# Performance work log

Hardware: AMD Instinct MI355X
Metric: run time of the kernel (lower is better)

## Reference

```python
import jax, jax.numpy as jnp
import numpy as np

EMB = 4096
NUM_EXPERTS = 64
TOP_K = 2
TOKENS = 16384


def setup_inputs() -> dict:
    key = jax.random.key(0)
    kx, kw, kb = jax.random.split(key, 3)
    x = jax.random.normal(kx, (TOKENS, EMB), dtype=jnp.float32)
    # nn.Linear(emb_size, num_experts): weight [num_experts, emb], bias [num_experts]
    W = jax.random.normal(kw, (NUM_EXPERTS, EMB), dtype=jnp.float32) / np.sqrt(EMB)
    b = jax.random.normal(kb, (NUM_EXPERTS,), dtype=jnp.float32) * 0.01
    return {"x": x, "W": W, "b": b}


def reference(x, W, b):
    # logits = x @ W.T + b  -> [tokens, num_experts]
    logits = jnp.einsum("td,ed->te", x, W) + b
    topk_val, topk_idx = jax.lax.top_k(logits, TOP_K)  # [tokens, k]
    probs = jax.nn.softmax(topk_val, axis=-1)
    return (topk_idx, probs)
```

## Files before the change

### kernel.cpp

```cpp
#include <hip/hip_runtime.h>

#define TOKENS 16384
#define EMB 4096
#define NEXP 64
#define BK 32
#define KSP 4
#define KPER (EMB / KSP)
#define NCH (KPER / BK)

typedef __attribute__((ext_vector_type(8))) short short8;
typedef __attribute__((ext_vector_type(4))) float f32x4;
typedef __attribute__((ext_vector_type(4))) unsigned short ush4;

#define WP_USHORTS (3 * NEXP * EMB)
#define WP_FLOATS  (WP_USHORTS / 2)

__device__ __forceinline__ void gl_lds16(const void* g, void* lds) {
    __builtin_amdgcn_global_load_lds(
        (const __attribute__((address_space(1))) void*)g,
        (__attribute__((address_space(3))) void*)lds, 16, 0, 0);
}

__device__ __forceinline__ void split3(float x, unsigned short& h,
                                       unsigned short& m, unsigned short& l) {
    unsigned u = __float_as_uint(x);
    unsigned r = u + 0x7FFFu + ((u >> 16) & 1u);
    float hF = __uint_as_float(r & 0xFFFF0000u);
    h = (unsigned short)(r >> 16);
    float r1 = x - hF;
    unsigned u1 = __float_as_uint(r1);
    float mF = __uint_as_float(u1 & 0xFFFF0000u);
    m = (unsigned short)(u1 >> 16);
    float r2 = r1 - mF;
    l = (unsigned short)(__float_as_uint(r2) >> 16);
}

__device__ __forceinline__ void split3_pair(float x0, float x1,
        unsigned& hw, unsigned& mw, unsigned& lw) {
    unsigned u0 = __float_as_uint(x0), u1 = __float_as_uint(x1);
    unsigned r0 = u0 + 0x7FFFu + ((u0 >> 16) & 1u);
    unsigned r1 = u1 + 0x7FFFu + ((u1 >> 16) & 1u);
    hw = __builtin_amdgcn_perm(r1, r0, 0x07060302u);
    float s0 = x0 - __uint_as_float(r0 & 0xFFFF0000u);
    float s1 = x1 - __uint_as_float(r1 & 0xFFFF0000u);
    unsigned v0 = __float_as_uint(s0), v1 = __float_as_uint(s1);
    mw = __builtin_amdgcn_perm(v1, v0, 0x07060302u);
    float t0 = s0 - __uint_as_float(v0 & 0xFFFF0000u);
    float t1 = s1 - __uint_as_float(v1 & 0xFFFF0000u);
    lw = __builtin_amdgcn_perm(__float_as_uint(t1), __float_as_uint(t0), 0x07060302u);
}

__device__ __forceinline__ void build_frags(const float4& a0, const float4& a1,
        short8& H, short8& M, short8& L) {
    union { short8 v; unsigned u[4]; } h_, m_, l_;
    split3_pair(a0.x, a0.y, h_.u[0], m_.u[0], l_.u[0]);
    split3_pair(a0.z, a0.w, h_.u[1], m_.u[1], l_.u[1]);
    split3_pair(a1.x, a1.y, h_.u[2], m_.u[2], l_.u[2]);
    split3_pair(a1.z, a1.w, h_.u[3], m_.u[3], l_.u[3]);
    H = h_.v; M = m_.v; L = l_.v;
}

__global__ __launch_bounds__(256) void split_w(const float* __restrict__ W,
                                               unsigned short* __restrict__ Wp) {
    const int i = (blockIdx.x * 256 + threadIdx.x) * 4;
    const float4 v = *reinterpret_cast<const float4*>(W + i);
    ush4 h, m, l;
#pragma unroll
    for (int e = 0; e < 4; ++e) {
        unsigned short he, me, le;
        split3(reinterpret_cast<const float*>(&v)[e], he, me, le);
        h[e] = he; m[e] = me; l[e] = le;
    }
    *reinterpret_cast<ush4*>(Wp + i) = h;
    *reinterpret_cast<ush4*>(Wp + NEXP * EMB + i) = m;
    *reinterpret_cast<ush4*>(Wp + 2 * NEXP * EMB + i) = l;
}

#define MFMA_BLOCK(BUFC, AH0, AM0, AL0, AH1, AM1, AL1)                          \
    _Pragma("unroll")                                                           \
    for (int et = 0; et < 4; ++et) {                                            \
        const unsigned short* bp = &sB[g][BUFC][et * 16 + lr][lo * 8];          \
        const short8 bH = *reinterpret_cast<const short8*>(bp);                 \
        const short8 bM = *reinterpret_cast<const short8*>(bp + 64 * BK);       \
        const short8 bL = *reinterpret_cast<const short8*>(bp + 128 * BK);      \
        accH[0][et] = __builtin_amdgcn_mfma_f32_16x16x32_bf16(AH0, bH, accH[0][et], 0, 0, 0); \
        accL[0][et] = __builtin_amdgcn_mfma_f32_16x16x32_bf16(AH0, bM, accL[0][et], 0, 0, 0); \
        accL[0][et] = __builtin_amdgcn_mfma_f32_16x16x32_bf16(AM0, bH, accL[0][et], 0, 0, 0); \
        accL[0][et] = __builtin_amdgcn_mfma_f32_16x16x32_bf16(AM0, bM, accL[0][et], 0, 0, 0); \
        accL[0][et] = __builtin_amdgcn_mfma_f32_16x16x32_bf16(AH0, bL, accL[0][et], 0, 0, 0); \
        accL[0][et] = __builtin_amdgcn_mfma_f32_16x16x32_bf16(AL0, bH, accL[0][et], 0, 0, 0); \
        accH[1][et] = __builtin_amdgcn_mfma_f32_16x16x32_bf16(AH1, bH, accH[1][et], 0, 0, 0); \
        accL[1][et] = __builtin_amdgcn_mfma_f32_16x16x32_bf16(AH1, bM, accL[1][et], 0, 0, 0); \
        accL[1][et] = __builtin_amdgcn_mfma_f32_16x16x32_bf16(AM1, bH, accL[1][et], 0, 0, 0); \
        accL[1][et] = __builtin_amdgcn_mfma_f32_16x16x32_bf16(AM1, bM, accL[1][et], 0, 0, 0); \
        accL[1][et] = __builtin_amdgcn_mfma_f32_16x16x32_bf16(AH1, bL, accL[1][et], 0, 0, 0); \
        accL[1][et] = __builtin_amdgcn_mfma_f32_16x16x32_bf16(AL1, bH, accL[1][et], 0, 0, 0); \
    }

#define BODY(KS, AC, BUFC) do {                                                 \
    asm volatile("s_waitcnt vmcnt(4)" ::: "memory");                            \
    __builtin_amdgcn_s_barrier();                                               \
    _Pragma("unroll")                                                           \
    for (int p = 0; p < 6; ++p)                                                 \
        gl_lds16(gb[p] + ((KS) + 1) * BK,                                       \
                 &sB[g][(BUFC) ^ 1][16 * (6 * h + p)][0]);                      \
    __builtin_amdgcn_sched_barrier(0);                                          \
    short8 aH0, aM0, aL0, aH1, aM1, aL1;                                        \
    build_frags(AC[0][0], AC[0][1], aH0, aM0, aL0);                             \
    build_frags(AC[1][0], AC[1][1], aH1, aM1, aL1);                             \
    _Pragma("unroll")                                                           \
    for (int ti = 0; ti < 2; ++ti) {                                            \
        AC[ti][0] = *reinterpret_cast<const float4*>(ax[ti] + ((KS) + 2) * BK);     \
        AC[ti][1] = *reinterpret_cast<const float4*>(ax[ti] + ((KS) + 2) * BK + 4); \
    }                                                                           \
    __builtin_amdgcn_sched_barrier(0);                                          \
    MFMA_BLOCK(BUFC, aH0, aM0, aL0, aH1, aM1, aL1)                              \
} while (0)

__global__ __launch_bounds__(512) void router_fused(
    const float* __restrict__ x, const unsigned short* __restrict__ Wp,
    const float* __restrict__ b, float* __restrict__ out)
{
    __shared__ unsigned short sB[KSP][2][192][BK];

    const int t  = threadIdx.x;
    const int w  = t >> 6;
    const int l  = t & 63;
    const int g  = w >> 1;
    const int h  = w & 1;
    const int lr = l & 15;
    const int lo = l >> 4;
    const int tokB = blockIdx.x * 64;
    const int tok0 = tokB + h * 32;
    const int kb   = g * KPER;

    const float* ax[2];
    ax[0] = x + (size_t)(tok0 + lr) * EMB + kb + lo * 8;
    ax[1] = ax[0] + (size_t)16 * EMB;

    const unsigned short* gb[6];
#pragma unroll
    for (int p = 0; p < 6; ++p)
        gb[p] = Wp + (size_t)(16 * (6 * h + p) + (l >> 2)) * EMB + kb + 8 * (l & 3);

    f32x4 accH[2][4], accL[2][4];
#pragma unroll
    for (int ti = 0; ti < 2; ++ti)
#pragma unroll
        for (int et = 0; et < 4; ++et) {
            accH[ti][et] = (f32x4){0.f, 0.f, 0.f, 0.f};
            accL[ti][et] = (f32x4){0.f, 0.f, 0.f, 0.f};
        }

    float4 aA[2][2], aB[2][2];
#pragma unroll
    for (int ti = 0; ti < 2; ++ti) {
        aA[ti][0] = *reinterpret_cast<const float4*>(ax[ti]);
        aA[ti][1] = *reinterpret_cast<const float4*>(ax[ti] + 4);
    }
    __builtin_amdgcn_sched_barrier(0);
#pragma unroll
    for (int p = 0; p < 6; ++p)
        gl_lds16(gb[p], &sB[g][0][16 * (6 * h + p)][0]);
    __builtin_amdgcn_sched_barrier(0);
#pragma unroll
    for (int ti = 0; ti < 2; ++ti) {
        aB[ti][0] = *reinterpret_cast<const float4*>(ax[ti] + BK);
        aB[ti][1] = *reinterpret_cast<const float4*>(ax[ti] + BK + 4);
    }
    __builtin_amdgcn_sched_barrier(0);

#pragma unroll 1
    for (int kt = 0; kt < NCH - 2; kt += 2) {
        BODY(kt, aA, 0);
        BODY(kt + 1, aB, 1);
    }
    {
        asm volatile("s_waitcnt vmcnt(4)" ::: "memory");
        __builtin_amdgcn_s_barrier();
#pragma unroll
        for (int p = 0; p < 6; ++p)
            gl_lds16(gb[p] + (NCH - 1) * BK, &sB[g][1][16 * (6 * h + p)][0]);
        __builtin_amdgcn_sched_barrier(0);
        short8 aH0, aM0, aL0, aH1, aM1, aL1;
        build_frags(aA[0][0], aA[0][1], aH0, aM0, aL0);
        build_frags(aA[1][0], aA[1][1], aH1, aM1, aL1);
        MFMA_BLOCK(0, aH0, aM0, aL0, aH1, aM1, aL1)
    }
    {
        asm volatile("s_waitcnt vmcnt(0)" ::: "memory");
        __builtin_amdgcn_s_barrier();
        short8 aH0, aM0, aL0, aH1, aM1, aL1;
        build_frags(aB[0][0], aB[0][1], aH0, aM0, aL0);
        build_frags(aB[1][0], aB[1][1], aH1, aM1, aL1);
        MFMA_BLOCK(1, aH0, aM0, aL0, aH1, aM1, aL1)
    }

    __syncthreads();
    float* logits = reinterpret_cast<float*>(&sB[0][0][0][0]);
#pragma unroll
    for (int ti = 0; ti < 2; ++ti)
#pragma unroll
        for (int et = 0; et < 4; ++et)
#pragma unroll
            for (int j = 0; j < 4; ++j) {
                const int ltok = h * 32 + ti * 16 + lo * 4 + j;
                logits[(g * 64 + ltok) * 65 + et * 16 + lr]
                    = accH[ti][et][j] + accL[ti][et][j];
            }
    __syncthreads();

    double* sv = reinterpret_cast<double*>(logits + KSP * 64 * 65);
    int*    si = reinterpret_cast<int*>(sv + 64 * 8 * 2);

    const int tok  = t >> 3;
    const int part = t & 7;
    double v[8];
#pragma unroll
    for (int j = 0; j < 8; ++j) v[j] = 0.0;
#pragma unroll
    for (int gg = 0; gg < KSP; ++gg)
#pragma unroll
        for (int j = 0; j < 8; ++j)
            v[j] += (double)logits[(gg * 64 + tok) * 65 + part * 8 + j];
#pragma unroll
    for (int j = 0; j < 8; ++j) v[j] += (double)b[part * 8 + j];

    double v1 = -1e300, v2 = -1e300; int i1 = 0, i2 = 0;
#pragma unroll
    for (int j = 0; j < 8; ++j) {
        const int e = part * 8 + j;
        if (v[j] > v1)      { v2 = v1; i2 = i1; v1 = v[j]; i1 = e; }
        else if (v[j] > v2) { v2 = v[j]; i2 = e; }
    }
    sv[(tok * 8 + part) * 2 + 0] = v1;
    sv[(tok * 8 + part) * 2 + 1] = v2;
    si[(tok * 8 + part) * 2 + 0] = i1;
    si[(tok * 8 + part) * 2 + 1] = i2;
    __syncthreads();

    if (part == 0) {
        double m1 = -1e300, m2 = -1e300; int j1 = 0, j2 = 0;
#pragma unroll
        for (int p = 0; p < 8; ++p)
#pragma unroll
            for (int r = 0; r < 2; ++r) {
                const double vv = sv[(tok * 8 + p) * 2 + r];
                const int    ii = si[(tok * 8 + p) * 2 + r];
                if (vv > m1)      { m2 = m1; j2 = j1; m1 = vv; j1 = ii; }
                else if (vv > m2) { m2 = vv; j2 = ii; }
            }
        const float e2  = expf((float)(m2 - m1));
        const float inv = 1.0f / (1.0f + e2);
        const int gt = tokB + tok;
        out[2 * gt]     = (float)j1;
        out[2 * gt + 1] = (float)j2;
        out[2 * TOKENS + 2 * gt]     = inv;
        out[2 * TOKENS + 2 * gt + 1] = e2 * inv;
    }
}

extern "C" void kernel_launch(void* const* d_in, const int* in_sizes, int n_in,
                              void* d_out, int out_size, void* d_ws, size_t ws_size,
                              hipStream_t stream) {
    const float* x = (const float*)d_in[0];
    const float* W = (const float*)d_in[1];
    const float* b = (const float*)d_in[2];
    float* out = (float*)d_out;
    unsigned short* Wp = (unsigned short*)d_ws;

    split_w<<<dim3(NEXP * EMB / 1024), dim3(256), 0, stream>>>(W, Wp);
    router_fused<<<dim3(TOKENS / 64), dim3(512), 0, stream>>>(x, Wp, b, out);
}
```

Measured before the change: 76.48 us.

## Split x into bf16 triples cooperatively via swizzled LDS instead of per-wave registers

Each block now loads x tiles of 128 columns with coalesced float4 reads, splits each element once into hi/mid/lo bf16 parts, and stores them to a swizzled LDS buffer. The K-split groups then read their MFMA fragments from LDS. The W layout is also changed so the four groups interleave 32-column slices within each 128-chunk instead of owning contiguous quarters. This is meant to make the x reads more coalesced and spread the split arithmetic across all threads, at the cost of two barriers per iteration, extra LDS traffic and full vmcnt(0) waits that reduce load/compute overlap.

Measured after the change: 89.19 us. +16.6%, slower.

```diff
diff --git a/kernel.cpp b/kernel.cpp
--- a/kernel.cpp
+++ b/kernel.cpp
@@ -3,10 +3,10 @@
 #define TOKENS 16384
 #define EMB 4096
 #define NEXP 64
-#define BK 32
 #define KSP 4
-#define KPER (EMB / KSP)
-#define NCH (KPER / BK)
+#define MK 128
+#define NM (EMB / MK)
+#define BKG 32
 
 typedef __attribute__((ext_vector_type(8))) short short8;
 typedef __attribute__((ext_vector_type(4))) float f32x4;
@@ -50,16 +50,6 @@
     lw = __builtin_amdgcn_perm(__float_as_uint(t1), __float_as_uint(t0), 0x07060302u);
 }
 
-__device__ __forceinline__ void build_frags(const float4& a0, const float4& a1,
-        short8& H, short8& M, short8& L) {
-    union { short8 v; unsigned u[4]; } h_, m_, l_;
-    split3_pair(a0.x, a0.y, h_.u[0], m_.u[0], l_.u[0]);
-    split3_pair(a0.z, a0.w, h_.u[1], m_.u[1], l_.u[1]);
-    split3_pair(a1.x, a1.y, h_.u[2], m_.u[2], l_.u[2]);
-    split3_pair(a1.z, a1.w, h_.u[3], m_.u[3], l_.u[3]);
-    H = h_.v; M = m_.v; L = l_.v;
-}
-
 __global__ __launch_bounds__(256) void split_w(const float* __restrict__ W,
                                                unsigned short* __restrict__ Wp) {
     const int i = (blockIdx.x * 256 + threadIdx.x) * 4;
@@ -76,52 +66,12 @@
     *reinterpret_cast<ush4*>(Wp + 2 * NEXP * EMB + i) = l;
 }
 
-#define MFMA_BLOCK(BUFC, AH0, AM0, AL0, AH1, AM1, AL1)                          \
-    _Pragma("unroll")                                                           \
-    for (int et = 0; et < 4; ++et) {                                            \
-        const unsigned short* bp = &sB[g][BUFC][et * 16 + lr][lo * 8];          \
-        const short8 bH = *reinterpret_cast<const short8*>(bp);                 \
-        const short8 bM = *reinterpret_cast<const short8*>(bp + 64 * BK);       \
-        const short8 bL = *reinterpret_cast<const short8*>(bp + 128 * BK);      \
-        accH[0][et] = __builtin_amdgcn_mfma_f32_16x16x32_bf16(AH0, bH, accH[0][et], 0, 0, 0); \
-        accL[0][et] = __builtin_amdgcn_mfma_f32_16x16x32_bf16(AH0, bM, accL[0][et], 0, 0, 0); \
-        accL[0][et] = __builtin_amdgcn_mfma_f32_16x16x32_bf16(AM0, bH, accL[0][et], 0, 0, 0); \
-        accL[0][et] = __builtin_amdgcn_mfma_f32_16x16x32_bf16(AM0, bM, accL[0][et], 0, 0, 0); \
-        accL[0][et] = __builtin_amdgcn_mfma_f32_16x16x32_bf16(AH0, bL, accL[0][et], 0, 0, 0); \
-        accL[0][et] = __builtin_amdgcn_mfma_f32_16x16x32_bf16(AL0, bH, accL[0][et], 0, 0, 0); \
-        accH[1][et] = __builtin_amdgcn_mfma_f32_16x16x32_bf16(AH1, bH, accH[1][et], 0, 0, 0); \
-        accL[1][et] = __builtin_amdgcn_mfma_f32_16x16x32_bf16(AH1, bM, accL[1][et], 0, 0, 0); \
-        accL[1][et] = __builtin_amdgcn_mfma_f32_16x16x32_bf16(AM1, bH, accL[1][et], 0, 0, 0); \
-        accL[1][et] = __builtin_amdgcn_mfma_f32_16x16x32_bf16(AM1, bM, accL[1][et], 0, 0, 0); \
-        accL[1][et] = __builtin_amdgcn_mfma_f32_16x16x32_bf16(AH1, bL, accL[1][et], 0, 0, 0); \
-        accL[1][et] = __builtin_amdgcn_mfma_f32_16x16x32_bf16(AL1, bH, accL[1][et], 0, 0, 0); \
-    }
-
-#define BODY(KS, AC, BUFC) do {                                                 \
-    asm volatile("s_waitcnt vmcnt(4)" ::: "memory");                            \
-    __builtin_amdgcn_s_barrier();                                               \
-    _Pragma("unroll")                                                           \
-    for (int p = 0; p < 6; ++p)                                                 \
-        gl_lds16(gb[p] + ((KS) + 1) * BK,                                       \
-                 &sB[g][(BUFC) ^ 1][16 * (6 * h + p)][0]);                      \
-    __builtin_amdgcn_sched_barrier(0);                                          \
-    short8 aH0, aM0, aL0, aH1, aM1, aL1;                                        \
-    build_frags(AC[0][0], AC[0][1], aH0, aM0, aL0);                             \
-    build_frags(AC[1][0], AC[1][1], aH1, aM1, aL1);                             \
-    _Pragma("unroll")                                                           \
-    for (int ti = 0; ti < 2; ++ti) {                                            \
-        AC[ti][0] = *reinterpret_cast<const float4*>(ax[ti] + ((KS) + 2) * BK);     \
-        AC[ti][1] = *reinterpret_cast<const float4*>(ax[ti] + ((KS) + 2) * BK + 4); \
-    }                                                                           \
-    __builtin_amdgcn_sched_barrier(0);                                          \
-    MFMA_BLOCK(BUFC, aH0, aM0, aL0, aH1, aM1, aL1)                              \
-} while (0)
-
-__global__ __launch_bounds__(512) void router_fused(
+__global__ __launch_bounds__(512, 1) void router_fused(
     const float* __restrict__ x, const unsigned short* __restrict__ Wp,
     const float* __restrict__ b, float* __restrict__ out)
 {
-    __shared__ unsigned short sB[KSP][2][192][BK];
+    __shared__ __align__(16) unsigned short sA[3 * 64 * MK];
+    __shared__ __align__(16) unsigned short sB[KSP][2][192][BKG];
 
     const int t  = threadIdx.x;
     const int w  = t >> 6;
@@ -131,17 +81,21 @@
     const int lr = l & 15;
     const int lo = l >> 4;
     const int tokB = blockIdx.x * 64;
-    const int tok0 = tokB + h * 32;
-    const int kb   = g * KPER;
-
-    const float* ax[2];
-    ax[0] = x + (size_t)(tok0 + lr) * EMB + kb + lo * 8;
-    ax[1] = ax[0] + (size_t)16 * EMB;
+
+    const float* axj[4];
+#pragma unroll
+    for (int j = 0; j < 4; ++j)
+        axj[j] = x + (size_t)(tokB + 16 * j + (t >> 5)) * EMB + (t & 31) * 4;
+
+    unsigned* sAu = reinterpret_cast<unsigned*>(sA);
+    const int swzW = ((t & 31) >> 1) ^ ((t >> 5) & 7);
+    const int wbase0 = (t >> 5) * 64 + swzW * 4 + (t & 1) * 2;
 
     const unsigned short* gb[6];
 #pragma unroll
     for (int p = 0; p < 6; ++p)
-        gb[p] = Wp + (size_t)(16 * (6 * h + p) + (l >> 2)) * EMB + kb + 8 * (l & 3);
+        gb[p] = Wp + (size_t)(16 * (6 * h + p) + (l >> 2)) * EMB
+              + g * BKG + 8 * (l & 3);
 
     f32x4 accH[2][4], accL[2][4];
 #pragma unroll
@@ -152,48 +106,76 @@
             accL[ti][et] = (f32x4){0.f, 0.f, 0.f, 0.f};
         }
 
-    float4 aA[2][2], aB[2][2];
-#pragma unroll
-    for (int ti = 0; ti < 2; ++ti) {
-        aA[ti][0] = *reinterpret_cast<const float4*>(ax[ti]);
-        aA[ti][1] = *reinterpret_cast<const float4*>(ax[ti] + 4);
-    }
-    __builtin_amdgcn_sched_barrier(0);
 #pragma unroll
     for (int p = 0; p < 6; ++p)
         gl_lds16(gb[p], &sB[g][0][16 * (6 * h + p)][0]);
-    __builtin_amdgcn_sched_barrier(0);
-#pragma unroll
-    for (int ti = 0; ti < 2; ++ti) {
-        aB[ti][0] = *reinterpret_cast<const float4*>(ax[ti] + BK);
-        aB[ti][1] = *reinterpret_cast<const float4*>(ax[ti] + BK + 4);
-    }
-    __builtin_amdgcn_sched_barrier(0);
+    float4 ar[4];
+#pragma unroll
+    for (int j = 0; j < 4; ++j)
+        ar[j] = *reinterpret_cast<const float4*>(axj[j]);
 
 #pragma unroll 1
-    for (int kt = 0; kt < NCH - 2; kt += 2) {
-        BODY(kt, aA, 0);
-        BODY(kt + 1, aB, 1);
-    }
-    {
-        asm volatile("s_waitcnt vmcnt(4)" ::: "memory");
-        __builtin_amdgcn_s_barrier();
-#pragma unroll
-        for (int p = 0; p < 6; ++p)
-            gl_lds16(gb[p] + (NCH - 1) * BK, &sB[g][1][16 * (6 * h + p)][0]);
-        __builtin_amdgcn_sched_barrier(0);
-        short8 aH0, aM0, aL0, aH1, aM1, aL1;
-        build_frags(aA[0][0], aA[0][1], aH0, aM0, aL0);
-        build_frags(aA[1][0], aA[1][1], aH1, aM1, aL1);
-        MFMA_BLOCK(0, aH0, aM0, aL0, aH1, aM1, aL1)
-    }
-    {
+    for (int m = 0; m < NM; ++m) {
+        const int buf = m & 1;
         asm volatile("s_waitcnt vmcnt(0)" ::: "memory");
         __builtin_amdgcn_s_barrier();
-        short8 aH0, aM0, aL0, aH1, aM1, aL1;
-        build_frags(aB[0][0], aB[0][1], aH0, aM0, aL0);
-        build_frags(aB[1][0], aB[1][1], aH1, aM1, aL1);
-        MFMA_BLOCK(1, aH0, aM0, aL0, aH1, aM1, aL1)
+        __builtin_amdgcn_sched_barrier(0);
+
+        if (m + 1 < NM) {
+#pragma unroll
+            for (int p = 0; p < 6; ++p)
+                gl_lds16(gb[p] + (m + 1) * MK,
+                         &sB[g][buf ^ 1][16 * (6 * h + p)][0]);
+        }
+#pragma unroll
+        for (int j = 0; j < 4; ++j) {
+            const float4 f = ar[j];
+            unsigned hw0, mw0, lw0, hw1, mw1, lw1;
+            split3_pair(f.x, f.y, hw0, mw0, lw0);
+            split3_pair(f.z, f.w, hw1, mw1, lw1);
+            const int rb = 16 * j * 64 + wbase0;
+            *reinterpret_cast<unsigned long long*>(sAu + rb)
+                = ((unsigned long long)hw1 << 32) | hw0;
+            *reinterpret_cast<unsigned long long*>(sAu + 4096 + rb)
+                = ((unsigned long long)mw1 << 32) | mw0;
+            *reinterpret_cast<unsigned long long*>(sAu + 8192 + rb)
+                = ((unsigned long long)lw1 << 32) | lw0;
+        }
+        if (m + 1 < NM) {
+#pragma unroll
+            for (int j = 0; j < 4; ++j)
+                ar[j] = *reinterpret_cast<const float4*>(axj[j] + (m + 1) * MK);
+        }
+        asm volatile("s_waitcnt lgkmcnt(0)" ::: "memory");
+        __builtin_amdgcn_s_barrier();
+        __builtin_amdgcn_sched_barrier(0);
+
+        short8 fr[2][3];
+#pragma unroll
+        for (int ti = 0; ti < 2; ++ti) {
+            const int tok = h * 32 + ti * 16 + lr;
+            const int o   = (g * 4 + lo) ^ (lr & 7);
+            const unsigned short* pa = sA + tok * MK + o * 8;
+            fr[ti][0] = *reinterpret_cast<const short8*>(pa);
+            fr[ti][1] = *reinterpret_cast<const short8*>(pa + 8192);
+            fr[ti][2] = *reinterpret_cast<const short8*>(pa + 16384);
+        }
+#pragma unroll
+        for (int et = 0; et < 4; ++et) {
+            const unsigned short* bp = &sB[g][buf][et * 16 + lr][lo * 8];
+            const short8 bH = *reinterpret_cast<const short8*>(bp);
+            const short8 bM = *reinterpret_cast<const short8*>(bp + 64 * BKG);
+            const short8 bL = *reinterpret_cast<const short8*>(bp + 128 * BKG);
+#pragma unroll
+            for (int ti = 0; ti < 2; ++ti) {
+                accH[ti][et] = __builtin_amdgcn_mfma_f32_16x16x32_bf16(fr[ti][0], bH, accH[ti][et], 0, 0, 0);
+                accL[ti][et] = __builtin_amdgcn_mfma_f32_16x16x32_bf16(fr[ti][0], bM, accL[ti][et], 0, 0, 0);
+                accL[ti][et] = __builtin_amdgcn_mfma_f32_16x16x32_bf16(fr[ti][1], bH, accL[ti][et], 0, 0, 0);
+                accL[ti][et] = __builtin_amdgcn_mfma_f32_16x16x32_bf16(fr[ti][1], bM, accL[ti][et], 0, 0, 0);
+                accL[ti][et] = __builtin_amdgcn_mfma_f32_16x16x32_bf16(fr[ti][0], bL, accL[ti][et], 0, 0, 0);
+                accL[ti][et] = __builtin_amdgcn_mfma_f32_16x16x32_bf16(fr[ti][2], bH, accL[ti][et], 0, 0, 0);
+            }
+        }
     }
 
     __syncthreads();
```

## Triple-buffer W tiles in LDS and prefetch x two chunks ahead

Applied to the files above, without the earlier changes.

Replaces the double-buffered LDS pipeline for W with a three-buffer rotation and loads x activations in pairs of chunks one macro-step ahead, issuing the next B chunk after the barrier so that two chunks of loads stay in flight during the MFMA work. The aim is to hide global-load latency better and cut barrier stalls in the K loop. In exchange it uses more LDS (three buffers per K-split group), doubles the A register staging, and depends on hand-tuned vmcnt counts that must match the exact number of outstanding loads.

Result: slower. 85.65 us (+12.0%).

```diff
diff --git a/kernel.cpp b/kernel.cpp
--- a/kernel.cpp
+++ b/kernel.cpp
@@ -7,6 +7,7 @@
 #define KSP 4
 #define KPER (EMB / KSP)
 #define NCH (KPER / BK)
+#define NMM (NCH / 2)
 
 typedef __attribute__((ext_vector_type(8))) short short8;
 typedef __attribute__((ext_vector_type(4))) float f32x4;
@@ -97,31 +98,51 @@
         accL[1][et] = __builtin_amdgcn_mfma_f32_16x16x32_bf16(AL1, bH, accL[1][et], 0, 0, 0); \
     }
 
-#define BODY(KS, AC, BUFC) do {                                                 \
-    asm volatile("s_waitcnt vmcnt(4)" ::: "memory");                            \
-    __builtin_amdgcn_s_barrier();                                               \
+#define ISSUE_B(CHUNK, BUF)                                                     \
     _Pragma("unroll")                                                           \
     for (int p = 0; p < 6; ++p)                                                 \
-        gl_lds16(gb[p] + ((KS) + 1) * BK,                                       \
-                 &sB[g][(BUFC) ^ 1][16 * (6 * h + p)][0]);                      \
-    __builtin_amdgcn_sched_barrier(0);                                          \
-    short8 aH0, aM0, aL0, aH1, aM1, aL1;                                        \
-    build_frags(AC[0][0], AC[0][1], aH0, aM0, aL0);                             \
-    build_frags(AC[1][0], AC[1][1], aH1, aM1, aL1);                             \
+        gl_lds16(gb[p] + (CHUNK) * BK, &sB[g][BUF][16 * (6 * h + p)][0]);
+
+#define ISSUE_A(MACRO, ASET)                                                    \
     _Pragma("unroll")                                                           \
     for (int ti = 0; ti < 2; ++ti) {                                            \
-        AC[ti][0] = *reinterpret_cast<const float4*>(ax[ti] + ((KS) + 2) * BK);     \
-        AC[ti][1] = *reinterpret_cast<const float4*>(ax[ti] + ((KS) + 2) * BK + 4); \
-    }                                                                           \
-    __builtin_amdgcn_sched_barrier(0);                                          \
+        const float* ab_ = ax[ti] + 2 * (MACRO) * BK;                           \
+        ASET[ti][0][0] = *reinterpret_cast<const float4*>(ab_);                 \
+        ASET[ti][0][1] = *reinterpret_cast<const float4*>(ab_ + 4);             \
+        ASET[ti][1][0] = *reinterpret_cast<const float4*>(ab_ + BK);            \
+        ASET[ti][1][1] = *reinterpret_cast<const float4*>(ab_ + BK + 4);        \
+    }
+
+#define COMPUTE(ASET, CI, BUFC) do {                                            \
+    short8 aH0, aM0, aL0, aH1, aM1, aL1;                                        \
+    build_frags(ASET[0][CI][0], ASET[0][CI][1], aH0, aM0, aL0);                 \
+    build_frags(ASET[1][CI][0], ASET[1][CI][1], aH1, aM1, aL1);                 \
     MFMA_BLOCK(BUFC, aH0, aM0, aL0, aH1, aM1, aL1)                              \
+} while (0)
+
+#define BODY(MM, ACUR, ANXT, BC0, BC1, BC2, ISLAST) do {                        \
+    ISSUE_B(2 * (MM) + 1, BC1);                                         \
+    if (!(ISLAST)) { ISSUE_A((MM) + 1, ANXT); }                         \
+    __builtin_amdgcn_sched_barrier(0);                                          \
+    if (ISLAST) asm volatile("s_waitcnt vmcnt(6)" ::: "memory");        \
+    else        asm volatile("s_waitcnt vmcnt(14)" ::: "memory");               \
+    __builtin_amdgcn_s_barrier();                                       \
+    __builtin_amdgcn_sched_barrier(0);                                          \
+    COMPUTE(ACUR, 0, BC0);                                              \
+    if (!(ISLAST)) { ISSUE_B(2 * (MM) + 2, BC2); }                      \
+    __builtin_amdgcn_sched_barrier(0);                                          \
+    if (ISLAST) asm volatile("s_waitcnt vmcnt(0)" ::: "memory");        \
+    else        asm volatile("s_waitcnt vmcnt(14)" ::: "memory");               \
+    __builtin_amdgcn_s_barrier();                                       \
+    __builtin_amdgcn_sched_barrier(0);                                          \
+    COMPUTE(ACUR, 1, BC1);                                              \
 } while (0)
 
 __global__ __launch_bounds__(512) void router_fused(
     const float* __restrict__ x, const unsigned short* __restrict__ Wp,
     const float* __restrict__ b, float* __restrict__ out)
 {
-    __shared__ unsigned short sB[KSP][2][192][BK];
+    __shared__ unsigned short sB[KSP][3][192][BK];
 
     const int t  = threadIdx.x;
     const int w  = t >> 6;
@@ -152,49 +173,25 @@
             accL[ti][et] = (f32x4){0.f, 0.f, 0.f, 0.f};
         }
 
-    float4 aA[2][2], aB[2][2];
-#pragma unroll
-    for (int ti = 0; ti < 2; ++ti) {
-        aA[ti][0] = *reinterpret_cast<const float4*>(ax[ti]);
-        aA[ti][1] = *reinterpret_cast<const float4*>(ax[ti] + 4);
-    }
+    float4 aA[2][2][2], aB[2][2][2];
+    ISSUE_A(0, aA);
     __builtin_amdgcn_sched_barrier(0);
-#pragma unroll
-    for (int p = 0; p < 6; ++p)
-        gl_lds16(gb[p], &sB[g][0][16 * (6 * h + p)][0]);
+    ISSUE_B(0, 0);
     __builtin_amdgcn_sched_barrier(0);
-#pragma unroll
-    for (int ti = 0; ti < 2; ++ti) {
-        aB[ti][0] = *reinterpret_cast<const float4*>(ax[ti] + BK);
-        aB[ti][1] = *reinterpret_cast<const float4*>(ax[ti] + BK + 4);
-    }
-    __builtin_amdgcn_sched_barrier(0);
 
 #pragma unroll 1
-    for (int kt = 0; kt < NCH - 2; kt += 2) {
-        BODY(kt, aA, 0);
-        BODY(kt + 1, aB, 1);
-    }
-    {
-        asm volatile("s_waitcnt vmcnt(4)" ::: "memory");
-        __builtin_amdgcn_s_barrier();
-#pragma unroll
-        for (int p = 0; p < 6; ++p)
-            gl_lds16(gb[p] + (NCH - 1) * BK, &sB[g][1][16 * (6 * h + p)][0]);
-        __builtin_amdgcn_sched_barrier(0);
-        short8 aH0, aM0, aL0, aH1, aM1, aL1;
-        build_frags(aA[0][0], aA[0][1], aH0, aM0, aL0);
-        build_frags(aA[1][0], aA[1][1], aH1, aM1, aL1);
-        MFMA_BLOCK(0, aH0, aM0, aL0, aH1, aM1, aL1)
-    }
-    {
-        asm volatile("s_waitcnt vmcnt(0)" ::: "memory");
-        __builtin_amdgcn_s_barrier();
-        short8 aH0, aM0, aL0, aH1, aM1, aL1;
-        build_frags(aB[0][0], aB[0][1], aH0, aM0, aL0);
-        build_frags(aB[1][0], aB[1][1], aH1, aM1, aL1);
-        MFMA_BLOCK(1, aH0, aM0, aL0, aH1, aM1, aL1)
-    }
+    for (int mb = 0; mb < 12; mb += 6) {
+        BODY(mb + 0, aA, aB, 0, 1, 2, false);
+        BODY(mb + 1, aB, aA, 2, 0, 1, false);
+        BODY(mb + 2, aA, aB, 1, 2, 0, false);
+        BODY(mb + 3, aB, aA, 0, 1, 2, false);
+        BODY(mb + 4, aA, aB, 2, 0, 1, false);
+        BODY(mb + 5, aB, aA, 1, 2, 0, false);
+    }
+    BODY(12, aA, aB, 0, 1, 2, false);
+    BODY(13, aB, aA, 2, 0, 1, false);
+    BODY(14, aA, aB, 1, 2, 0, false);
+    BODY(15, aB, aA, 0, 1, 2, true);
 
     __syncthreads();
     float* logits = reinterpret_cast<float*>(&sB[0][0][0][0]);
```
